# Optimization experiments

Measured on AMD Instinct MI355X. Metric: run time of the kernel, lower is better.

The kernel has to match this reference:

```python
import jax, jax.numpy as jnp
import numpy as np

TOP_K = 2  # num_experts_per_tok


def setup_inputs() -> dict:
    key = jax.random.key(0)
    ks = jax.random.split(key, 7)
    B, S, D = 4, 4096, 512
    E, H = 16, 4 * 512  # num_experts, expert hidden dim
    s_in = 1.0 / np.sqrt(D)
    s_h = 1.0 / np.sqrt(H)
    return {
        "x": jax.random.normal(ks[0], (B, S, D), dtype=jnp.float32),
        "Wg": jax.random.normal(ks[1], (D, E), dtype=jnp.float32) * s_in,
        "bg": jnp.zeros((E,), dtype=jnp.float32),
        "W1": jax.random.normal(ks[2], (E, D, H), dtype=jnp.float32) * s_in,
        "b1": jnp.zeros((E, H), dtype=jnp.float32),
        "W2": jax.random.normal(ks[3], (E, H, D), dtype=jnp.float32) * s_h,
        "b2": jnp.zeros((E, D), dtype=jnp.float32),
    }


def reference(x, Wg, bg, W1, b1, W2, b2):
    B, S, D = x.shape
    E = W1.shape[0]
    xf = x.reshape(-1, D)  # [T, D], T = B*S

    # 1. routing: top-k gate logits, softmax over the selected k (in fp32)
    logits = xf @ Wg + bg                      # [T, E]
    w, idx = jax.lax.top_k(logits, TOP_K)      # [T, K]
    w = jax.nn.softmax(w.astype(jnp.float32), axis=1).astype(x.dtype)

    # 2. combine weights per (token, expert): sum of gate weights where selected
    onehot = jax.nn.one_hot(idx, E, dtype=x.dtype)   # [T, K, E]
    combine = jnp.einsum("tk,tke->te", w, onehot)    # [T, E]

    # 3. per-expert FFN (Linear -> GELU(exact) -> Linear), masked combine.
    # Fixed loop over experts (structural, not data dim); tokens not routed to
    # expert e get combine weight 0, matching the sort/segment/scatter original.
    out = jnp.zeros_like(xf)
    for e in range(E):
        h = jax.nn.gelu(xf @ W1[e] + b1[e], approximate=False)  # [T, H]
        y = h @ W2[e] + b2[e]                                   # [T, D]
        out = out + combine[:, e:e + 1] * y

    return out.reshape(B, S, D)
```

## Files before the change

### kernel.cpp

```cpp
#include <hip/hip_runtime.h>
#include <hip/hip_bf16.h>

#define T_TOK 16384
#define DDIM  512
#define NEXP  16
#define HDIM  2048
#define NSLOT (T_TOK * 2)
#define NHB   128

#define GBM 128
#define GBN 256
#define GBN2 128
#define BK  32
#define MAXTILE 272
#define TSLICE  136

typedef __attribute__((ext_vector_type(8))) short short8;
typedef __attribute__((ext_vector_type(4))) short short4v;
typedef __attribute__((ext_vector_type(4))) float f32x4;

__device__ inline short f2bf(float f) {
    __hip_bfloat16 h = __float2bfloat16(f);
    return *reinterpret_cast<short*>(&h);
}
__device__ inline float bf2f(short s) {
    unsigned u = ((unsigned)(unsigned short)s) << 16;
    union { unsigned u; float f; } c; c.u = u; return c.f;
}
__device__ inline float erf_fast(float x) {
    float ax = fabsf(x);
    float t = 1.0f / fmaf(0.3275911f, ax, 1.0f);
    float p = fmaf(fmaf(fmaf(fmaf(1.061405429f, t, -1.453152027f), t,
                  1.421413741f), t, -0.284496736f), t, 0.254829592f) * t;
    float r = 1.0f - p * __expf(-ax * ax);
    return copysignf(r, x);
}
__device__ inline float geluf(float v) {
    return 0.5f * v * (1.0f + erf_fast(v * 0.70710678118654752440f));
}
__device__ inline void gload16(const void* g, void* l) {
    __builtin_amdgcn_global_load_lds(
        (const __attribute__((address_space(1))) void*)g,
        (__attribute__((address_space(3))) void*)l, 16, 0, 0);
}
__device__ inline void xcd_decode(int lin, int nx, int tc, int& y, int& xn) {
    if ((tc & 7) == 0) {
        int tpx = tc >> 3;
        int k = lin & 7, j = lin >> 3;
        y = k * tpx + j % tpx;
        xn = j / tpx;
    } else {
        xn = lin % nx;
        y = lin / nx;
    }
}

__global__ __launch_bounds__(256) void gate_kernel(
    const float* __restrict__ x, const float* __restrict__ wg,
    const float* __restrict__ bg, int* __restrict__ tok_e,
    float* __restrict__ tok_w)
{
    int wv = threadIdx.x >> 6, lane = threadIdx.x & 63;
    int t = blockIdx.x * 4 + wv;
    int g = lane >> 4, q = lane & 15;
    const float* xr = x + (size_t)t * DDIM + g * 128;
    const float* wr = wg + (size_t)g * 128 * NEXP + q;
    double a0 = 0, a1 = 0, a2 = 0, a3 = 0;
#pragma unroll
    for (int c = 0; c < 8; ++c) {
        float4 v0 = ((const float4*)xr)[c * 4 + 0];
        float4 v1 = ((const float4*)xr)[c * 4 + 1];
        float4 v2 = ((const float4*)xr)[c * 4 + 2];
        float4 v3 = ((const float4*)xr)[c * 4 + 3];
        const float* wp = wr + c * 16 * NEXP;
        a0 += (double)v0.x * (double)wp[0 * NEXP];
        a1 += (double)v0.y * (double)wp[1 * NEXP];
        a2 += (double)v0.z * (double)wp[2 * NEXP];
        a3 += (double)v0.w * (double)wp[3 * NEXP];
        a0 += (double)v1.x * (double)wp[4 * NEXP];
        a1 += (double)v1.y * (double)wp[5 * NEXP];
        a2 += (double)v1.z * (double)wp[6 * NEXP];
        a3 += (double)v1.w * (double)wp[7 * NEXP];
        a0 += (double)v2.x * (double)wp[8 * NEXP];
        a1 += (double)v2.y * (double)wp[9 * NEXP];
        a2 += (double)v2.z * (double)wp[10 * NEXP];
        a3 += (double)v2.w * (double)wp[11 * NEXP];
        a0 += (double)v3.x * (double)wp[12 * NEXP];
        a1 += (double)v3.y * (double)wp[13 * NEXP];
        a2 += (double)v3.z * (double)wp[14 * NEXP];
        a3 += (double)v3.w * (double)wp[15 * NEXP];
    }
    double a = ((a0 + a1) + (a2 + a3));
    a += __shfl_xor(a, 16, 64);
    a += __shfl_xor(a, 32, 64);
    a += (double)bg[q];
    double v0 = a; int i0 = q;
#pragma unroll
    for (int s = 1; s < 16; s <<= 1) {
        double ov = __shfl_xor(v0, s, 64);
        int oi = __shfl_xor(i0, s, 64);
        if (ov > v0 || (ov == v0 && oi < i0)) { v0 = ov; i0 = oi; }
    }
    double m2 = (q == i0) ? -1e300 : a;
    double v1 = m2; int i1 = q;
#pragma unroll
    for (int s = 1; s < 16; s <<= 1) {
        double ov = __shfl_xor(v1, s, 64);
        int oi = __shfl_xor(i1, s, 64);
        if (ov > v1 || (ov == v1 && oi < i1)) { v1 = ov; i1 = oi; }
    }
    if (lane == 0) {
        float ex = expf((float)(v1 - v0));
        float w0 = 1.0f / (1.0f + ex);
        tok_e[2 * t] = i0; tok_e[2 * t + 1] = i1;
        tok_w[2 * t] = w0; tok_w[2 * t + 1] = ex * w0;
    }
}

__global__ __launch_bounds__(256) void hist_kernel(
    const int* __restrict__ tok_e, int* __restrict__ bhist)
{
    __shared__ int h[NEXP];
    if (threadIdx.x < NEXP) h[threadIdx.x] = 0;
    __syncthreads();
    atomicAdd(&h[tok_e[blockIdx.x * 256 + threadIdx.x]], 1);
    __syncthreads();
    if (threadIdx.x < NEXP) bhist[blockIdx.x * NEXP + threadIdx.x] = h[threadIdx.x];
}

__global__ void scan_kernel(const int* __restrict__ bhist, int* __restrict__ offs,
                            int* __restrict__ bbase, int* __restrict__ tile_e,
                            int* __restrict__ tile_m0)
{
    int tid = threadIdx.x;
    __shared__ int tot[NEXP];
    if (tid < NEXP) {
        int s = 0;
        for (int b = 0; b < NHB; ++b) s += bhist[b * NEXP + tid];
        tot[tid] = s;
    }
    __syncthreads();
    if (tid == 0) {
        int run = 0;
        for (int e = 0; e < NEXP; ++e) { offs[e] = run; run += tot[e]; }
        offs[NEXP] = run;
        int nt = 0;
        for (int e = 0; e < NEXP; ++e)
            for (int m = offs[e]; m < offs[e + 1]; m += GBM) {
                tile_e[nt] = e; tile_m0[nt] = m; ++nt;
            }
        offs[17] = nt;
    }
    __syncthreads();
    if (tid < NEXP) {
        int run = offs[tid];
        for (int b = 0; b < NHB; ++b) {
            bbase[b * NEXP + tid] = run;
            run += bhist[b * NEXP + tid];
        }
    }
}

__global__ __launch_bounds__(256) void scatter_kernel(
    const int* __restrict__ tok_e, const float* __restrict__ tok_w,
    const int* __restrict__ bbase, int* __restrict__ list_tok,
    float* __restrict__ list_w, int* __restrict__ pos_tk)
{
    __shared__ int h[NEXP];
    if (threadIdx.x < NEXP) h[threadIdx.x] = 0;
    __syncthreads();
    int s = blockIdx.x * 256 + threadIdx.x;
    int e = tok_e[s];
    int r = atomicAdd(&h[e], 1);
    int pos = bbase[blockIdx.x * NEXP + e] + r;
    list_tok[pos] = s >> 1;
    list_w[pos] = tok_w[s];
    pos_tk[s] = pos;
}


__global__ void cvt_bf16_kernel(const float* __restrict__ src, short* __restrict__ dst, int n4)
{
    int i = blockIdx.x * blockDim.x + threadIdx.x;
    int stride = gridDim.x * blockDim.x;
    for (; i < n4; i += stride) {
        float4 v = ((const float4*)src)[i];
        short4v o;
        o[0] = f2bf(v.x); o[1] = f2bf(v.y); o[2] = f2bf(v.z); o[3] = f2bf(v.w);
        ((short4v*)dst)[i] = o;
    }
}

__global__ void wtrans_kernel(const float* __restrict__ src, short* __restrict__ dst, int R, int C)
{
    __shared__ float t[32][33];
    int c0 = blockIdx.x * 32, r0 = blockIdx.y * 32;
    const float* s = src + (size_t)blockIdx.z * R * C;
    short* d = dst + (size_t)blockIdx.z * R * C;
    int cc = threadIdx.x & 31, rr = threadIdx.x >> 5;
#pragma unroll
    for (int pp = 0; pp < 4; ++pp)
        t[rr + pp * 8][cc] = s[(size_t)(r0 + rr + pp * 8) * C + c0 + cc];
    __syncthreads();
#pragma unroll
    for (int pp = 0; pp < 4; ++pp) {
        int c = rr + pp * 8;
        d[(size_t)(c0 + c) * R + r0 + cc] = f2bf(t[cc][c]);
    }
}


__global__ __launch_bounds__(512) void gemm1_kernel(
    const short* __restrict__ xbf, const short* __restrict__ w1t,
    const float* __restrict__ b1, const int* __restrict__ offs,
    const int* __restrict__ tile_e, const int* __restrict__ tile_m0,
    const int* __restrict__ list_tok, short* __restrict__ hbuf,
    int h0, int hlen, int t0, int tc)
{
    int ty, xn;
    xcd_decode((int)blockIdx.x, hlen / GBN, tc, ty, xn);
    int tb = t0 + ty;
    if (tb >= offs[17]) return;
    int e = tile_e[tb], m0 = tile_m0[tb];
    int rows = offs[e + 1] - m0; if (rows > GBM) rows = GBM;
    int n0 = xn * GBN;
    int tid = threadIdx.x, l = tid & 63, w = tid >> 6;

    __shared__ __align__(16) short As[2][GBM * BK];
    __shared__ __align__(16) short Bs[2][GBN * BK];
    __shared__ int ts[GBM];
    if (tid < GBM) ts[tid] = list_tok[m0 + (tid < rows ? tid : rows - 1)];
    __syncthreads();

    int arow = w * 16 + (l >> 2);
    int aslot = (l & 3) ^ ((arow >> 1) & 3);
    const short* gA = xbf + (size_t)ts[arow] * DDIM + aslot * 8;
    int brow0 = (w * 2 + 0) * 16 + (l >> 2);
    int brow1 = (w * 2 + 1) * 16 + (l >> 2);
    int bs0 = (l & 3) ^ ((brow0 >> 1) & 3);
    int bs1 = (l & 3) ^ ((brow1 >> 1) & 3);
    const short* gB0 = w1t + ((size_t)e * HDIM + (size_t)(h0 + n0 + brow0)) * DDIM + bs0 * 8;
    const short* gB1 = w1t + ((size_t)e * HDIM + (size_t)(h0 + n0 + brow1)) * DDIM + bs1 * 8;

    int l15 = l & 15, kq = l >> 4;
    int aoff[4], boff[4];
#pragma unroll
    for (int mi = 0; mi < 4; ++mi) {
        int R = (w >> 2) * 64 + mi * 16 + l15;
        aoff[mi] = R * BK + ((kq ^ ((R >> 1) & 3)) * 8);
    }
#pragma unroll
    for (int ni = 0; ni < 4; ++ni) {
        int S = (w & 3) * 64 + ni * 16 + l15;
        boff[ni] = S * BK + ((kq ^ ((S >> 1) & 3)) * 8);
    }

    f32x4 vzero = {0.0f, 0.0f, 0.0f, 0.0f};
    f32x4 acc[4][4];
#pragma unroll
    for (int i = 0; i < 4; ++i)
#pragma unroll
        for (int j = 0; j < 4; ++j) acc[i][j] = vzero;

#define STAGE1(T, B) {                                            \
        gload16(gA  + (T) * BK, &As[B][w * 512]);                 \
        gload16(gB0 + (T) * BK, &Bs[B][(w * 2 + 0) * 512]);       \
        gload16(gB1 + (T) * BK, &Bs[B][(w * 2 + 1) * 512]); }

    const int nt = DDIM / BK;
    STAGE1(0, 0);
    asm volatile("s_waitcnt vmcnt(0)" ::: "memory");
    __builtin_amdgcn_s_barrier();
#pragma unroll 1
    for (int t = 0; t < nt; ++t) {
        int cur = t & 1;
        if (t + 1 < nt) STAGE1(t + 1, cur ^ 1);
        __builtin_amdgcn_sched_barrier(0);
        const short* Ab = &As[cur][0];
        const short* Bb = &Bs[cur][0];
        short8 af[4], bv[4];
#pragma unroll
        for (int mi = 0; mi < 4; ++mi) af[mi] = *(const short8*)(Ab + aoff[mi]);
#pragma unroll
        for (int ni = 0; ni < 4; ++ni) bv[ni] = *(const short8*)(Bb + boff[ni]);
        __builtin_amdgcn_s_setprio(1);
#pragma unroll
        for (int mi = 0; mi < 4; ++mi)
#pragma unroll
            for (int ni = 0; ni < 4; ++ni)
                acc[mi][ni] = __builtin_amdgcn_mfma_f32_16x16x32_bf16(
                    af[mi], bv[ni], acc[mi][ni], 0, 0, 0);
        __builtin_amdgcn_s_setprio(0);
        if (t + 1 < nt) {
            asm volatile("s_waitcnt vmcnt(0)" ::: "memory");
            __builtin_amdgcn_s_barrier();
        }
    }
#undef STAGE1

    int crow = (w >> 2) * 64 + (kq << 2);
    int ccol = (w & 3) * 64 + l15;
#pragma unroll
    for (int mi = 0; mi < 4; ++mi) {
#pragma unroll
        for (int ni = 0; ni < 4; ++ni) {
            int col = ccol + ni * 16;
            float bias = b1[e * HDIM + h0 + n0 + col];
#pragma unroll
            for (int j = 0; j < 4; ++j) {
                int row = crow + mi * 16 + j;
                if (row < rows) {
                    float v = acc[mi][ni][j] + bias;
                    hbuf[(size_t)(m0 + row) * hlen + (n0 + col)] = f2bf(geluf(v));
                }
            }
        }
    }
}

__global__ __launch_bounds__(512) void gemm2_kernel(
    const short* __restrict__ hbuf, const short* __restrict__ w2t,
    const float* __restrict__ b2, const int* __restrict__ offs,
    const int* __restrict__ tile_e, const int* __restrict__ tile_m0,
    const int* __restrict__ list_tok, const float* __restrict__ list_w,
    short* __restrict__ ybuf, float* __restrict__ out,
    int h0, int hlen, int mode, int t0, int tc)
{
    int ty, xn;
    xcd_decode((int)blockIdx.x, DDIM / GBN2, tc, ty, xn);
    int tb = t0 + ty;
    if (tb >= offs[17]) return;
    int e = tile_e[tb], m0 = tile_m0[tb];
    int rows = offs[e + 1] - m0; if (rows > GBM) rows = GBM;
    int n0 = xn * GBN2;
    int tid = threadIdx.x, l = tid & 63, w = tid >> 6;

    __shared__ __align__(16) short As[2][GBM * BK];
    __shared__ __align__(16) short Bs[2][GBN2 * BK];
    __shared__ int ts[GBM];
    __shared__ float lw[GBM];
    if (tid < GBM) {
        int idx = m0 + (tid < rows ? tid : rows - 1);
        ts[tid] = list_tok[idx];
        lw[tid] = list_w[idx];
    }
    __syncthreads();

    int arow = w * 16 + (l >> 2);
    int aslot = (l & 3) ^ ((arow >> 1) & 3);
    int aslotg = m0 + arow; if (aslotg >= NSLOT) aslotg = NSLOT - 1;
    const short* gA = hbuf + (size_t)aslotg * hlen + aslot * 8;
    int brow = w * 16 + (l >> 2);
    int bslot = (l & 3) ^ ((brow >> 1) & 3);
    const short* gB = w2t + ((size_t)e * DDIM + (size_t)(n0 + brow)) * HDIM + h0 + bslot * 8;

    int l15 = l & 15, kq = l >> 4;
    int aoff[4], boff[2];
#pragma unroll
    for (int mi = 0; mi < 4; ++mi) {
        int R = (w >> 2) * 64 + mi * 16 + l15;
        aoff[mi] = R * BK + ((kq ^ ((R >> 1) & 3)) * 8);
    }
#pragma unroll
    for (int ni = 0; ni < 2; ++ni) {
        int S = (w & 3) * 32 + ni * 16 + l15;
        boff[ni] = S * BK + ((kq ^ ((S >> 1) & 3)) * 8);
    }

    f32x4 vzero = {0.0f, 0.0f, 0.0f, 0.0f};
    f32x4 acc[4][2];
#pragma unroll
    for (int i = 0; i < 4; ++i)
#pragma unroll
        for (int j = 0; j < 2; ++j) acc[i][j] = vzero;

#define STAGE2(T, B) {                                            \
        gload16(gA + (T) * BK, &As[B][w * 512]);                  \
        gload16(gB + (T) * BK, &Bs[B][w * 512]); }

    const int nt = hlen / BK;
    STAGE2(0, 0);
    asm volatile("s_waitcnt vmcnt(0)" ::: "memory");
    __builtin_amdgcn_s_barrier();
#pragma unroll 1
    for (int t = 0; t < nt; ++t) {
        int cur = t & 1;
        if (t + 1 < nt) STAGE2(t + 1, cur ^ 1);
        __builtin_amdgcn_sched_barrier(0);
        const short* Ab = &As[cur][0];
        const short* Bb = &Bs[cur][0];
        short8 af[4], bv[2];
#pragma unroll
        for (int mi = 0; mi < 4; ++mi) af[mi] = *(const short8*)(Ab + aoff[mi]);
#pragma unroll
        for (int ni = 0; ni < 2; ++ni) bv[ni] = *(const short8*)(Bb + boff[ni]);
        __builtin_amdgcn_s_setprio(1);
#pragma unroll
        for (int mi = 0; mi < 4; ++mi)
#pragma unroll
            for (int ni = 0; ni < 2; ++ni)
                acc[mi][ni] = __builtin_amdgcn_mfma_f32_16x16x32_bf16(
                    af[mi], bv[ni], acc[mi][ni], 0, 0, 0);
        __builtin_amdgcn_s_setprio(0);
        if (t + 1 < nt) {
            asm volatile("s_waitcnt vmcnt(0)" ::: "memory");
            __builtin_amdgcn_s_barrier();
        }
    }
#undef STAGE2

    int crow = (w >> 2) * 64 + (kq << 2);
    int ccol = (w & 3) * 32 + l15;
#pragma unroll
    for (int mi = 0; mi < 4; ++mi) {
#pragma unroll
        for (int ni = 0; ni < 2; ++ni) {
            int col = ccol + ni * 16;
            float bias = (h0 == 0) ? b2[e * DDIM + n0 + col] : 0.0f;
#pragma unroll
            for (int j = 0; j < 4; ++j) {
                int row = crow + mi * 16 + j;
                if (row < rows) {
                    float v = acc[mi][ni][j] + bias;
                    if (mode == 0)
                        ybuf[(size_t)(m0 + row) * DDIM + n0 + col] = f2bf(v);
                    else
                        atomicAdd(&out[(size_t)ts[row] * DDIM + n0 + col], lw[row] * v);
                }
            }
        }
    }
}

__global__ __launch_bounds__(256) void combine_kernel(
    const short* __restrict__ ybuf, const int* __restrict__ pos_tk,
    const float* __restrict__ tok_w, float* __restrict__ out)
{
    int i = blockIdx.x * 256 + threadIdx.x;
    int t = i >> 6, c = (i & 63) * 8;
    float w0 = tok_w[2 * t], w1 = tok_w[2 * t + 1];
    int p0 = pos_tk[2 * t], p1 = pos_tk[2 * t + 1];
    short8 a = *(const short8*)(ybuf + (size_t)p0 * DDIM + c);
    short8 b = *(const short8*)(ybuf + (size_t)p1 * DDIM + c);
    float4 o0, o1;
    float* op = (float*)&o0;
#pragma unroll
    for (int j = 0; j < 4; ++j) op[j] = w0 * bf2f(a[j]) + w1 * bf2f(b[j]);
    float* op1 = (float*)&o1;
#pragma unroll
    for (int j = 0; j < 4; ++j) op1[j] = w0 * bf2f(a[4 + j]) + w1 * bf2f(b[4 + j]);
    float4* ob = (float4*)(out + (size_t)t * DDIM + c);
    ob[0] = o0;
    ob[1] = o1;
}


extern "C" void kernel_launch(void* const* d_in, const int* in_sizes, int n_in,
                              void* d_out, int out_size, void* d_ws, size_t ws_size,
                              hipStream_t stream)
{
    const float* x  = (const float*)d_in[0];
    const float* wg = (const float*)d_in[1];
    const float* bg = (const float*)d_in[2];
    const float* w1 = (const float*)d_in[3];
    const float* b1 = (const float*)d_in[4];
    const float* w2 = (const float*)d_in[5];
    const float* b2 = (const float*)d_in[6];
    float* out = (float*)d_out;

    char* p = (char*)d_ws;
    int* offs     = (int*)(p + 128);
    int* tile_e   = (int*)(p + 256);
    int* tile_m0  = (int*)(p + 2304);
    int* bhist    = (int*)(p + 8192);
    int* bbase    = (int*)(p + 16384);
    int* tok_e    = (int*)(p + 32768);
    float* tok_w  = (float*)(p + 32768 + 131072);
    int* list_tok = (int*)(p + 32768 + 262144);
    float* list_w = (float*)(p + 32768 + 393216);
    int* pos_tk   = (int*)(p + 32768 + 524288);
    short* xbf    = (short*)(p + 32768 + 655360);
    short* w1t    = xbf + (size_t)T_TOK * DDIM;
    short* w2t    = w1t + (size_t)NEXP * DDIM * HDIM;
    char* after   = (char*)(w2t + (size_t)NEXP * DDIM * HDIM);
    size_t fixed  = (size_t)(after - p);

    int mode, hlen = HDIM;
    if (fixed + (size_t)NSLOT * DDIM * 2 + (size_t)NSLOT * HDIM * 2 <= ws_size) {
        mode = 0;
    } else {
        mode = 1;
        hlen = 0;
        for (int hl = HDIM; hl >= 128; hl >>= 1)
            if (fixed + (size_t)NSLOT * hl * 2 <= ws_size) { hlen = hl; break; }
    }
    short* ybuf = (short*)after;
    short* hbuf = (mode == 0) ? (short*)(after + (size_t)NSLOT * DDIM * 2) : (short*)after;

    if (!hlen) { hipMemsetAsync(d_out, 0, (size_t)out_size * sizeof(float), stream); return; }
    if (mode == 1) hipMemsetAsync(d_out, 0, (size_t)out_size * sizeof(float), stream);

    gate_kernel<<<T_TOK / 4, 256, 0, stream>>>(x, wg, bg, tok_e, tok_w);
    hist_kernel<<<NHB, 256, 0, stream>>>(tok_e, bhist);
    scan_kernel<<<1, 64, 0, stream>>>(bhist, offs, bbase, tile_e, tile_m0);
    scatter_kernel<<<NHB, 256, 0, stream>>>(tok_e, tok_w, bbase, list_tok, list_w, pos_tk);
    cvt_bf16_kernel<<<2048, 256, 0, stream>>>(x, xbf, T_TOK * DDIM / 4);
    wtrans_kernel<<<dim3(HDIM / 32, DDIM / 32, NEXP), 256, 0, stream>>>(w1, w1t, DDIM, HDIM);
    wtrans_kernel<<<dim3(DDIM / 32, HDIM / 32, NEXP), 256, 0, stream>>>(w2, w2t, HDIM, DDIM);

    for (int h0 = 0; h0 < HDIM; h0 += hlen) {
        for (int t0 = 0; t0 < MAXTILE; t0 += TSLICE) {
            int tc = MAXTILE - t0; if (tc > TSLICE) tc = TSLICE;
            gemm1_kernel<<<(hlen / GBN) * tc, 512, 0, stream>>>(
                xbf, w1t, b1, offs, tile_e, tile_m0, list_tok, hbuf, h0, hlen, t0, tc);
            gemm2_kernel<<<(DDIM / GBN2) * tc, 512, 0, stream>>>(
                hbuf, w2t, b2, offs, tile_e, tile_m0, list_tok, list_w,
                ybuf, out, h0, hlen, mode, t0, tc);
        }
    }
    if (mode == 0)
        combine_kernel<<<T_TOK * 64 / 256, 256, 0, stream>>>(ybuf, pos_tk, tok_w, out);
}
```

Before: 397.9 us.

## Enlarge gemm1 tiles to 256x256 and split work by token halves

The first expert GEMM now uses 256-row by 256-column tiles with a separate 256-row tile list built in the scan kernel. Each warp computes a 128x64 sub-tile, so operand reuse from LDS rises. The two launch slices now split at the midpoint of the 256-row tile list, and a matching split point is found in the 128-row list for gemm2. The fixed grid sizes (80 and 160 tiles per slice) also change the XCD block mapping. In exchange, LDS use and accumulator registers double, which can lower occupancy, and the fixed grid caps may not cover every tile for skewed routing.

```diff
diff --git a/kernel.cpp b/kernel.cpp
--- a/kernel.cpp
+++ b/kernel.cpp
@@ -9,11 +9,10 @@
 #define NHB   128
 
 #define GBM 128
-#define GBN 256
 #define GBN2 128
 #define BK  32
-#define MAXTILE 272
-#define TSLICE  136
+#define G1TC 80
+#define G2TC 160
 
 typedef __attribute__((ext_vector_type(8))) short short8;
 typedef __attribute__((ext_vector_type(4))) short short4v;
@@ -43,16 +42,10 @@
         (const __attribute__((address_space(1))) void*)g,
         (__attribute__((address_space(3))) void*)l, 16, 0, 0);
 }
-__device__ inline void xcd_decode(int lin, int nx, int tc, int& y, int& xn) {
-    if ((tc & 7) == 0) {
-        int tpx = tc >> 3;
-        int k = lin & 7, j = lin >> 3;
-        y = k * tpx + j % tpx;
-        xn = j / tpx;
-    } else {
-        xn = lin % nx;
-        y = lin / nx;
-    }
+__device__ inline void xcd_decode(int lin, int tpx, int& y, int& xn) {
+    int k = lin & 7, j = lin >> 3;
+    y = (j % tpx) * 8 + k;
+    xn = j / tpx;
 }
 
 __global__ __launch_bounds__(256) void gate_kernel(
@@ -130,7 +123,8 @@
 
 __global__ void scan_kernel(const int* __restrict__ bhist, int* __restrict__ offs,
                             int* __restrict__ bbase, int* __restrict__ tile_e,
-                            int* __restrict__ tile_m0)
+                            int* __restrict__ tile_m0, int* __restrict__ t2e,
+                            int* __restrict__ t2m)
 {
     int tid = threadIdx.x;
     __shared__ int tot[NEXP];
@@ -150,6 +144,19 @@
                 tile_e[nt] = e; tile_m0[nt] = m; ++nt;
             }
         offs[17] = nt;
+        int n2 = 0;
+        for (int e = 0; e < NEXP; ++e)
+            for (int m = offs[e]; m < offs[e + 1]; m += 256) {
+                t2e[n2] = e; t2m[n2] = m; ++n2;
+            }
+        offs[18] = n2;
+        int c2 = n2 / 2;
+        offs[19] = c2;
+        int sc = (c2 < n2) ? t2m[c2] : offs[NEXP];
+        int c1 = nt;
+        for (int j = 0; j < nt; ++j)
+            if (tile_m0[j] == sc) { c1 = j; break; }
+        offs[20] = c1;
     }
     __syncthreads();
     if (tid < NEXP) {
@@ -213,59 +220,60 @@
 __global__ __launch_bounds__(512) void gemm1_kernel(
     const short* __restrict__ xbf, const short* __restrict__ w1t,
     const float* __restrict__ b1, const int* __restrict__ offs,
-    const int* __restrict__ tile_e, const int* __restrict__ tile_m0,
+    const int* __restrict__ t2e, const int* __restrict__ t2m,
     const int* __restrict__ list_tok, short* __restrict__ hbuf,
-    int h0, int hlen, int t0, int tc)
+    int h0, int hlen, int s)
 {
     int ty, xn;
-    xcd_decode((int)blockIdx.x, hlen / GBN, tc, ty, xn);
-    int tb = t0 + ty;
-    if (tb >= offs[17]) return;
-    int e = tile_e[tb], m0 = tile_m0[tb];
-    int rows = offs[e + 1] - m0; if (rows > GBM) rows = GBM;
-    int n0 = xn * GBN;
+    xcd_decode((int)blockIdx.x, G1TC / 8, ty, xn);
+    int lo = s ? offs[19] : 0;
+    int hi = s ? offs[18] : offs[19];
+    int tb = lo + ty;
+    if (tb >= hi) return;
+    int e = t2e[tb], m0 = t2m[tb];
+    int rows = offs[e + 1] - m0; if (rows > 256) rows = 256;
+    int n0 = xn * 256;
     int tid = threadIdx.x, l = tid & 63, w = tid >> 6;
 
-    __shared__ __align__(16) short As[2][GBM * BK];
-    __shared__ __align__(16) short Bs[2][GBN * BK];
-    __shared__ int ts[GBM];
-    if (tid < GBM) ts[tid] = list_tok[m0 + (tid < rows ? tid : rows - 1)];
-    __syncthreads();
-
-    int arow = w * 16 + (l >> 2);
-    int aslot = (l & 3) ^ ((arow >> 1) & 3);
-    const short* gA = xbf + (size_t)ts[arow] * DDIM + aslot * 8;
-    int brow0 = (w * 2 + 0) * 16 + (l >> 2);
-    int brow1 = (w * 2 + 1) * 16 + (l >> 2);
-    int bs0 = (l & 3) ^ ((brow0 >> 1) & 3);
-    int bs1 = (l & 3) ^ ((brow1 >> 1) & 3);
-    const short* gB0 = w1t + ((size_t)e * HDIM + (size_t)(h0 + n0 + brow0)) * DDIM + bs0 * 8;
-    const short* gB1 = w1t + ((size_t)e * HDIM + (size_t)(h0 + n0 + brow1)) * DDIM + bs1 * 8;
+    __shared__ __align__(16) short As[2][256 * BK];
+    __shared__ __align__(16) short Bs[2][256 * BK];
+    __shared__ int ts[256];
+    if (tid < 256) ts[tid] = list_tok[m0 + (tid < rows ? tid : rows - 1)];
+    __syncthreads();
+
+    int ar0 = w * 32 + (l >> 2), ar1 = ar0 + 16;
+    int as0 = (l & 3) ^ ((ar0 >> 1) & 3), as1 = (l & 3) ^ ((ar1 >> 1) & 3);
+    const short* gA0 = xbf + (size_t)ts[ar0] * DDIM + as0 * 8;
+    const short* gA1 = xbf + (size_t)ts[ar1] * DDIM + as1 * 8;
+    const short* gB0 = w1t + ((size_t)e * HDIM + (size_t)(h0 + n0 + ar0)) * DDIM + as0 * 8;
+    const short* gB1 = w1t + ((size_t)e * HDIM + (size_t)(h0 + n0 + ar1)) * DDIM + as1 * 8;
 
     int l15 = l & 15, kq = l >> 4;
-    int aoff[4], boff[4];
-#pragma unroll
-    for (int mi = 0; mi < 4; ++mi) {
-        int R = (w >> 2) * 64 + mi * 16 + l15;
+    int wm = w >> 2, wn = w & 3;
+    int aoff[8], boff[4];
+#pragma unroll
+    for (int mi = 0; mi < 8; ++mi) {
+        int R = wm * 128 + mi * 16 + l15;
         aoff[mi] = R * BK + ((kq ^ ((R >> 1) & 3)) * 8);
     }
 #pragma unroll
     for (int ni = 0; ni < 4; ++ni) {
-        int S = (w & 3) * 64 + ni * 16 + l15;
+        int S = wn * 64 + ni * 16 + l15;
         boff[ni] = S * BK + ((kq ^ ((S >> 1) & 3)) * 8);
     }
 
     f32x4 vzero = {0.0f, 0.0f, 0.0f, 0.0f};
-    f32x4 acc[4][4];
-#pragma unroll
-    for (int i = 0; i < 4; ++i)
+    f32x4 acc[8][4];
+#pragma unroll
+    for (int i = 0; i < 8; ++i)
 #pragma unroll
         for (int j = 0; j < 4; ++j) acc[i][j] = vzero;
 
 #define STAGE1(T, B) {                                            \
-        gload16(gA  + (T) * BK, &As[B][w * 512]);                 \
-        gload16(gB0 + (T) * BK, &Bs[B][(w * 2 + 0) * 512]);       \
-        gload16(gB1 + (T) * BK, &Bs[B][(w * 2 + 1) * 512]); }
+        gload16(gA0 + (T) * BK, &As[B][w * 1024]);                \
+        gload16(gA1 + (T) * BK, &As[B][w * 1024 + 512]);          \
+        gload16(gB0 + (T) * BK, &Bs[B][w * 1024]);                \
+        gload16(gB1 + (T) * BK, &Bs[B][w * 1024 + 512]); }
 
     const int nt = DDIM / BK;
     STAGE1(0, 0);
@@ -278,14 +286,14 @@
         __builtin_amdgcn_sched_barrier(0);
         const short* Ab = &As[cur][0];
         const short* Bb = &Bs[cur][0];
-        short8 af[4], bv[4];
-#pragma unroll
-        for (int mi = 0; mi < 4; ++mi) af[mi] = *(const short8*)(Ab + aoff[mi]);
+        short8 af[8], bv[4];
+#pragma unroll
+        for (int mi = 0; mi < 8; ++mi) af[mi] = *(const short8*)(Ab + aoff[mi]);
 #pragma unroll
         for (int ni = 0; ni < 4; ++ni) bv[ni] = *(const short8*)(Bb + boff[ni]);
         __builtin_amdgcn_s_setprio(1);
 #pragma unroll
-        for (int mi = 0; mi < 4; ++mi)
+        for (int mi = 0; mi < 8; ++mi)
 #pragma unroll
             for (int ni = 0; ni < 4; ++ni)
                 acc[mi][ni] = __builtin_amdgcn_mfma_f32_16x16x32_bf16(
@@ -298,10 +306,10 @@
     }
 #undef STAGE1
 
-    int crow = (w >> 2) * 64 + (kq << 2);
-    int ccol = (w & 3) * 64 + l15;
-#pragma unroll
-    for (int mi = 0; mi < 4; ++mi) {
+    int crow = wm * 128 + (kq << 2);
+    int ccol = wn * 64 + l15;
+#pragma unroll
+    for (int mi = 0; mi < 8; ++mi) {
 #pragma unroll
         for (int ni = 0; ni < 4; ++ni) {
             int col = ccol + ni * 16;
@@ -324,12 +332,14 @@
     const int* __restrict__ tile_e, const int* __restrict__ tile_m0,
     const int* __restrict__ list_tok, const float* __restrict__ list_w,
     short* __restrict__ ybuf, float* __restrict__ out,
-    int h0, int hlen, int mode, int t0, int tc)
+    int h0, int hlen, int mode, int s)
 {
     int ty, xn;
-    xcd_decode((int)blockIdx.x, DDIM / GBN2, tc, ty, xn);
-    int tb = t0 + ty;
-    if (tb >= offs[17]) return;
+    xcd_decode((int)blockIdx.x, G2TC / 8, ty, xn);
+    int lo = s ? offs[20] : 0;
+    int hi = s ? offs[17] : offs[20];
+    int tb = lo + ty;
+    if (tb >= hi) return;
     int e = tile_e[tb], m0 = tile_m0[tb];
     int rows = offs[e + 1] - m0; if (rows > GBM) rows = GBM;
     int n0 = xn * GBN2;
@@ -472,6 +482,8 @@
     int* offs     = (int*)(p + 128);
     int* tile_e   = (int*)(p + 256);
     int* tile_m0  = (int*)(p + 2304);
+    int* t2e      = (int*)(p + 4352);
+    int* t2m      = (int*)(p + 5376);
     int* bhist    = (int*)(p + 8192);
     int* bbase    = (int*)(p + 16384);
     int* tok_e    = (int*)(p + 32768);
@@ -491,7 +503,7 @@
     } else {
         mode = 1;
         hlen = 0;
-        for (int hl = HDIM; hl >= 128; hl >>= 1)
+        for (int hl = HDIM; hl >= 256; hl >>= 1)
             if (fixed + (size_t)NSLOT * hl * 2 <= ws_size) { hlen = hl; break; }
     }
     short* ybuf = (short*)after;
@@ -502,20 +514,19 @@
 
     gate_kernel<<<T_TOK / 4, 256, 0, stream>>>(x, wg, bg, tok_e, tok_w);
     hist_kernel<<<NHB, 256, 0, stream>>>(tok_e, bhist);
-    scan_kernel<<<1, 64, 0, stream>>>(bhist, offs, bbase, tile_e, tile_m0);
+    scan_kernel<<<1, 64, 0, stream>>>(bhist, offs, bbase, tile_e, tile_m0, t2e, t2m);
     scatter_kernel<<<NHB, 256, 0, stream>>>(tok_e, tok_w, bbase, list_tok, list_w, pos_tk);
     cvt_bf16_kernel<<<2048, 256, 0, stream>>>(x, xbf, T_TOK * DDIM / 4);
     wtrans_kernel<<<dim3(HDIM / 32, DDIM / 32, NEXP), 256, 0, stream>>>(w1, w1t, DDIM, HDIM);
     wtrans_kernel<<<dim3(DDIM / 32, HDIM / 32, NEXP), 256, 0, stream>>>(w2, w2t, HDIM, DDIM);
 
     for (int h0 = 0; h0 < HDIM; h0 += hlen) {
-        for (int t0 = 0; t0 < MAXTILE; t0 += TSLICE) {
-            int tc = MAXTILE - t0; if (tc > TSLICE) tc = TSLICE;
-            gemm1_kernel<<<(hlen / GBN) * tc, 512, 0, stream>>>(
-                xbf, w1t, b1, offs, tile_e, tile_m0, list_tok, hbuf, h0, hlen, t0, tc);
-            gemm2_kernel<<<(DDIM / GBN2) * tc, 512, 0, stream>>>(
+        for (int s = 0; s < 2; ++s) {
+            gemm1_kernel<<<(hlen / 256) * G1TC, 512, 0, stream>>>(
+                xbf, w1t, b1, offs, t2e, t2m, list_tok, hbuf, h0, hlen, s);
+            gemm2_kernel<<<(DDIM / GBN2) * G2TC, 512, 0, stream>>>(
                 hbuf, w2t, b2, offs, tile_e, tile_m0, list_tok, list_w,
-                ybuf, out, h0, hlen, mode, t0, tc);
+                ybuf, out, h0, hlen, mode, s);
         }
     }
     if (mode == 0)
```

After: 493.2 us. 24.0% more time.

## Overlap gemm2 of first tile slice with gemm1 of second in one launch

Applied to the files above, without the earlier changes.

The expert GEMMs are split into two tile slices. Each gemm body now takes its shared-memory region and block index as arguments, so a merged mid_kernel can run gemm2 for slice 0 and gemm1 for slice 1 in the same grid. This aims to remove a launch boundary and fill the tail and idle CUs between the dependent GEMMs. The cost is that the merged kernel allocates the larger shared-memory footprint for every block, which may lower occupancy for the gemm2 blocks. The minimum hidden-chunk length for the low-memory fallback is also raised to 256.

```diff
diff --git a/kernel.cpp b/kernel.cpp
--- a/kernel.cpp
+++ b/kernel.cpp
@@ -14,6 +14,7 @@
 #define BK  32
 #define MAXTILE 272
 #define TSLICE  136
+#define G2BLK   (4 * TSLICE)
 
 typedef __attribute__((ext_vector_type(8))) short short8;
 typedef __attribute__((ext_vector_type(4))) short short4v;
@@ -210,15 +211,18 @@
 }
 
 
-__global__ __launch_bounds__(512) void gemm1_kernel(
+__device__ void gemm1_body(char* smem, int lin,
     const short* __restrict__ xbf, const short* __restrict__ w1t,
     const float* __restrict__ b1, const int* __restrict__ offs,
     const int* __restrict__ tile_e, const int* __restrict__ tile_m0,
     const int* __restrict__ list_tok, short* __restrict__ hbuf,
     int h0, int hlen, int t0, int tc)
 {
+    short (*As)[GBM * BK] = (short(*)[GBM * BK])smem;
+    short (*Bs)[GBN * BK] = (short(*)[GBN * BK])(smem + 16384);
+    int* ts = (int*)(smem + 49152);
     int ty, xn;
-    xcd_decode((int)blockIdx.x, hlen / GBN, tc, ty, xn);
+    xcd_decode(lin, hlen / GBN, tc, ty, xn);
     int tb = t0 + ty;
     if (tb >= offs[17]) return;
     int e = tile_e[tb], m0 = tile_m0[tb];
@@ -226,9 +230,6 @@
     int n0 = xn * GBN;
     int tid = threadIdx.x, l = tid & 63, w = tid >> 6;
 
-    __shared__ __align__(16) short As[2][GBM * BK];
-    __shared__ __align__(16) short Bs[2][GBN * BK];
-    __shared__ int ts[GBM];
     if (tid < GBM) ts[tid] = list_tok[m0 + (tid < rows ? tid : rows - 1)];
     __syncthreads();
 
@@ -318,7 +319,7 @@
     }
 }
 
-__global__ __launch_bounds__(512) void gemm2_kernel(
+__device__ void gemm2_body(char* smem, int lin,
     const short* __restrict__ hbuf, const short* __restrict__ w2t,
     const float* __restrict__ b2, const int* __restrict__ offs,
     const int* __restrict__ tile_e, const int* __restrict__ tile_m0,
@@ -326,8 +327,12 @@
     short* __restrict__ ybuf, float* __restrict__ out,
     int h0, int hlen, int mode, int t0, int tc)
 {
+    short (*As)[GBM * BK]  = (short(*)[GBM * BK])smem;
+    short (*Bs)[GBN2 * BK] = (short(*)[GBN2 * BK])(smem + 16384);
+    int* ts = (int*)(smem + 32768);
+    float* lw = (float*)(smem + 33280);
     int ty, xn;
-    xcd_decode((int)blockIdx.x, DDIM / GBN2, tc, ty, xn);
+    xcd_decode(lin, DDIM / GBN2, tc, ty, xn);
     int tb = t0 + ty;
     if (tb >= offs[17]) return;
     int e = tile_e[tb], m0 = tile_m0[tb];
@@ -335,10 +340,6 @@
     int n0 = xn * GBN2;
     int tid = threadIdx.x, l = tid & 63, w = tid >> 6;
 
-    __shared__ __align__(16) short As[2][GBM * BK];
-    __shared__ __align__(16) short Bs[2][GBN2 * BK];
-    __shared__ int ts[GBM];
-    __shared__ float lw[GBM];
     if (tid < GBM) {
         int idx = m0 + (tid < rows ? tid : rows - 1);
         ts[tid] = list_tok[idx];
@@ -430,6 +431,43 @@
             }
         }
     }
+}
+
+__global__ __launch_bounds__(512) void gemm1_kernel(
+    const short* xbf, const short* w1t, const float* b1, const int* offs,
+    const int* tile_e, const int* tile_m0, const int* list_tok, short* hbuf,
+    int h0, int hlen, int t0, int tc)
+{
+    __shared__ __align__(16) char smem[49664];
+    gemm1_body(smem, (int)blockIdx.x, xbf, w1t, b1, offs, tile_e, tile_m0,
+               list_tok, hbuf, h0, hlen, t0, tc);
+}
+
+__global__ __launch_bounds__(512) void gemm2_kernel(
+    const short* hbuf, const short* w2t, const float* b2, const int* offs,
+    const int* tile_e, const int* tile_m0, const int* list_tok,
+    const float* list_w, short* ybuf, float* out,
+    int h0, int hlen, int mode, int t0, int tc)
+{
+    __shared__ __align__(16) char smem[33792];
+    gemm2_body(smem, (int)blockIdx.x, hbuf, w2t, b2, offs, tile_e, tile_m0,
+               list_tok, list_w, ybuf, out, h0, hlen, mode, t0, tc);
+}
+
+__global__ __launch_bounds__(512) void mid_kernel(
+    const short* xbf, const short* w1t, const float* b1,
+    const short* hbuf, const short* w2t, const float* b2,
+    const int* offs, const int* tile_e, const int* tile_m0,
+    const int* list_tok, const float* list_w, short* ybuf, float* out,
+    int h0, int hlen, int mode)
+{
+    __shared__ __align__(16) char smem[49664];
+    if ((int)blockIdx.x < G2BLK)
+        gemm2_body(smem, (int)blockIdx.x, hbuf, w2t, b2, offs, tile_e, tile_m0,
+                   list_tok, list_w, ybuf, out, h0, hlen, mode, 0, TSLICE);
+    else
+        gemm1_body(smem, (int)blockIdx.x - G2BLK, xbf, w1t, b1, offs, tile_e,
+                   tile_m0, list_tok, (short*)hbuf, h0, hlen, TSLICE, TSLICE);
 }
 
 __global__ __launch_bounds__(256) void combine_kernel(
@@ -491,7 +529,7 @@
     } else {
         mode = 1;
         hlen = 0;
-        for (int hl = HDIM; hl >= 128; hl >>= 1)
+        for (int hl = HDIM; hl >= 256; hl >>= 1)
             if (fixed + (size_t)NSLOT * hl * 2 <= ws_size) { hlen = hl; break; }
     }
     short* ybuf = (short*)after;
@@ -509,14 +547,14 @@
     wtrans_kernel<<<dim3(DDIM / 32, HDIM / 32, NEXP), 256, 0, stream>>>(w2, w2t, HDIM, DDIM);
 
     for (int h0 = 0; h0 < HDIM; h0 += hlen) {
-        for (int t0 = 0; t0 < MAXTILE; t0 += TSLICE) {
-            int tc = MAXTILE - t0; if (tc > TSLICE) tc = TSLICE;
-            gemm1_kernel<<<(hlen / GBN) * tc, 512, 0, stream>>>(
-                xbf, w1t, b1, offs, tile_e, tile_m0, list_tok, hbuf, h0, hlen, t0, tc);
-            gemm2_kernel<<<(DDIM / GBN2) * tc, 512, 0, stream>>>(
-                hbuf, w2t, b2, offs, tile_e, tile_m0, list_tok, list_w,
-                ybuf, out, h0, hlen, mode, t0, tc);
-        }
+        gemm1_kernel<<<(hlen / GBN) * TSLICE, 512, 0, stream>>>(
+            xbf, w1t, b1, offs, tile_e, tile_m0, list_tok, hbuf, h0, hlen, 0, TSLICE);
+        mid_kernel<<<G2BLK + (hlen / GBN) * TSLICE, 512, 0, stream>>>(
+            xbf, w1t, b1, hbuf, w2t, b2, offs, tile_e, tile_m0,
+            list_tok, list_w, ybuf, out, h0, hlen, mode);
+        gemm2_kernel<<<(DDIM / GBN2) * TSLICE, 512, 0, stream>>>(
+            hbuf, w2t, b2, offs, tile_e, tile_m0, list_tok, list_w,
+            ybuf, out, h0, hlen, mode, TSLICE, TSLICE);
     }
     if (mode == 0)
         combine_kernel<<<T_TOK * 64 / 256, 256, 0, stream>>>(ybuf, pos_tk, tok_w, out);
```

After: 568.0 us. 1.43x slower.
